# Optimization experiments

Measured on AMD Instinct MI355X. Metric: run time of the kernel, lower is better.

## Reference

```python
import jax, jax.numpy as jnp
import numpy as np

N_NODES = 100000


def gcn_conv(x, W, b, src, dst, n_nodes):
    # PyG GCNConv: h = x @ W; out = D^-1/2 (A + I) D^-1/2 h + b
    h = x @ W  # [N, F_out]
    e_ones = jnp.ones(src.shape[0], dtype=x.dtype)
    deg = jax.ops.segment_sum(e_ones, dst, num_segments=n_nodes) + 1.0  # self-loop
    dinv = jax.lax.rsqrt(deg)  # [N]
    norm = dinv[src] * dinv[dst]  # [E]
    msg = h[src] * norm[:, None]  # [E, F_out] (memory-bound gather)
    agg = jax.ops.segment_sum(msg, dst, num_segments=n_nodes)
    agg = agg + h * (dinv * dinv)[:, None]  # self-loop contribution
    return agg + b


def setup_inputs() -> dict:
    key = jax.random.key(0)
    ks = jax.random.split(key, 9)
    in_dim, h1, h2, out_dim = 512, 256, 128, 64
    n_edges = 1_600_000
    x = jax.random.normal(ks[0], (N_NODES, in_dim), dtype=jnp.float32)
    edge_index = jax.random.randint(ks[1], (2, n_edges), 0, N_NODES, dtype=jnp.int32)
    def glorot(k, fi, fo):
        s = float(np.sqrt(6.0 / (fi + fo)))
        return jax.random.uniform(k, (fi, fo), jnp.float32, -s, s)
    return {
        "x": x,
        "edge_index": edge_index,
        "W1": glorot(ks[2], in_dim, h1), "b1": jnp.zeros((h1,), jnp.float32),
        "W2": glorot(ks[3], h1, h2), "b2": jnp.zeros((h2,), jnp.float32),
        "W3": glorot(ks[4], h2, out_dim), "b3": jnp.zeros((out_dim,), jnp.float32),
    }


def reference(x, edge_index, W1, b1, W2, b2, W3, b3):
    src, dst = edge_index[0], edge_index[1]
    h = gcn_conv(x, W1, b1, src, dst, N_NODES)
    h = jax.nn.relu(h)  # dropout omitted (eval mode)
    h = gcn_conv(h, W2, b2, src, dst, N_NODES)
    h = jax.nn.relu(h)
    h = gcn_conv(h, W3, b3, src, dst, N_NODES)
    return jax.nn.log_softmax(h, axis=1)
```

## Files before the change

### kernel.cpp

```cpp
#include <hip/hip_runtime.h>
#include <hip/hip_bf16.h>

#define NN 100000
#define MP 100096

typedef unsigned short u16;
typedef __attribute__((ext_vector_type(8))) short bf16x8;
typedef __attribute__((ext_vector_type(4))) float f32x4;

static inline size_t align_up(size_t x, size_t a) { return (x + a - 1) & ~(a - 1); }

__device__ inline u16 f2b(float f) {
    unsigned u = __float_as_uint(f);
    return (u16)((u + 0x7FFF + ((u >> 16) & 1)) >> 16);
}
__device__ inline float b2f(u16 u) { return __uint_as_float(((unsigned)u) << 16); }


__global__ __launch_bounds__(256) void deg_count_kernel(const int* __restrict__ dst,
                                                        int* __restrict__ deg, int E) {
    int t = blockIdx.x * 256 + threadIdx.x;
    if (t < E) atomicAdd(&deg[dst[t]], 1);
}

__global__ __launch_bounds__(256) void dinv_kernel(const int* __restrict__ deg,
                                                   float* __restrict__ dinv, int n) {
    int t = blockIdx.x * 256 + threadIdx.x;
    if (t < n) dinv[t] = rsqrtf((float)deg[t] + 1.0f);
}

__global__ __launch_bounds__(256) void scan_phase1(const int* __restrict__ deg,
                                                   int* __restrict__ partials, int n4) {
    __shared__ int red[256];
    const int t = threadIdx.x;
    const int g = blockIdx.x * 256 + t;
    int4 v = make_int4(0, 0, 0, 0);
    if (g < n4) v = ((const int4*)deg)[g];
    red[t] = v.x + v.y + v.z + v.w;
    __syncthreads();
    #pragma unroll
    for (int d = 128; d; d >>= 1) {
        if (t < d) red[t] += red[t + d];
        __syncthreads();
    }
    if (t == 0) partials[blockIdx.x] = red[0];
}

__global__ __launch_bounds__(128) void scan_phase2(int* __restrict__ partials,
                                                   int* __restrict__ rowptr, int nb, int n) {
    __shared__ int ps[128];
    const int t = threadIdx.x;
    int v = (t < nb) ? partials[t] : 0;
    ps[t] = v;
    __syncthreads();
    #pragma unroll
    for (int d = 1; d < 128; d <<= 1) {
        int u = (t >= d) ? ps[t - d] : 0;
        __syncthreads();
        ps[t] += u;
        __syncthreads();
    }
    if (t < nb) partials[t] = ps[t] - v;
    if (t == nb - 1) rowptr[n] = ps[t];
}

__global__ __launch_bounds__(256) void scan_phase3(const int* __restrict__ deg,
                                                   const int* __restrict__ partials,
                                                   int* __restrict__ rowptr, int n4) {
    __shared__ int ts[256];
    const int t = threadIdx.x;
    const int g = blockIdx.x * 256 + t;
    int4 v = make_int4(0, 0, 0, 0);
    if (g < n4) v = ((const int4*)deg)[g];
    const int s0 = v.x, s1 = s0 + v.y, s2 = s1 + v.z, s3 = s2 + v.w;
    ts[t] = s3;
    __syncthreads();
    #pragma unroll
    for (int d = 1; d < 256; d <<= 1) {
        int u = (t >= d) ? ts[t - d] : 0;
        __syncthreads();
        ts[t] += u;
        __syncthreads();
    }
    if (g < n4) {
        const int base = partials[blockIdx.x] + ts[t] - s3;
        int4 r;
        r.x = base; r.y = base + s0; r.z = base + s1; r.w = base + s2;
        ((int4*)rowptr)[g] = r;
    }
}

__global__ __launch_bounds__(256) void reorder_kernel(const int* __restrict__ src,
        const int* __restrict__ dst, const int* __restrict__ rowptr,
        int* __restrict__ cursor, const float* __restrict__ dinv,
        int2* __restrict__ erec, int E) {
    int e = blockIdx.x * 256 + threadIdx.x;
    if (e >= E) return;
    int s = src[e], d = dst[e];
    int pos = rowptr[d] + atomicAdd(&cursor[d], 1);
    erec[pos] = make_int2(s, __float_as_int(dinv[s] * dinv[d]));
}


__global__ __launch_bounds__(256) void transpose_kernel(const float* __restrict__ W,
                                                        u16* __restrict__ WT, int K, int N) {
    int t = blockIdx.x * 256 + threadIdx.x;
    if (t >= K * N) return;
    int n = t / K, k = t - n * K;
    WT[t] = f2b(W[(size_t)k * N + n]);
}

__global__ __launch_bounds__(256) void gemm_mfma(const u16* __restrict__ A,
        const u16* __restrict__ BT, u16* __restrict__ C, int K, int ldc) {
    __shared__ char lds[32768];
    char* Al = lds;
    char* Bl = lds + 16384;
    const int tid = threadIdx.x;
    const int l = tid & 63;
    const int w = tid >> 6;
    const int wm = w >> 1, wn = w & 1;
    const long bm = (long)blockIdx.x * 128;
    const long bn = (long)blockIdx.y * 128;

    f32x4 acc[4][4];
    #pragma unroll
    for (int mi = 0; mi < 4; ++mi)
        #pragma unroll
        for (int ni = 0; ni < 4; ++ni)
            acc[mi][ni] = (f32x4){0.f, 0.f, 0.f, 0.f};

    const int srow = tid >> 3;
    const int schunk = (tid & 7) << 4;

    for (int k0 = 0; k0 < K; k0 += 64) {
        __syncthreads();
        #pragma unroll
        for (int i = 0; i < 4; ++i) {
            const int row = i * 32 + srow;
            const int lb = schunk ^ ((row & 7) << 4);
            const u16* ga = A + (bm + row) * K + k0 + (lb >> 1);
            const u16* gb = BT + (bn + row) * K + k0 + (lb >> 1);
            char* la = Al + i * 4096 + tid * 16;
            char* lbp = Bl + i * 4096 + tid * 16;
            __builtin_amdgcn_global_load_lds((const __attribute__((address_space(1))) void*)ga,
                                             (__attribute__((address_space(3))) void*)la, 16, 0, 0);
            __builtin_amdgcn_global_load_lds((const __attribute__((address_space(1))) void*)gb,
                                             (__attribute__((address_space(3))) void*)lbp, 16, 0, 0);
        }
        __syncthreads();
        #pragma unroll
        for (int kk = 0; kk < 2; ++kk) {
            const int kbyte = kk * 64 + ((l >> 4) << 4);
            const int swz = (l & 7) << 4;
            bf16x8 af[4], bfr[4];
            #pragma unroll
            for (int mi = 0; mi < 4; ++mi) {
                const int row = wm * 64 + mi * 16 + (l & 15);
                af[mi] = *(const bf16x8*)(Al + row * 128 + (kbyte ^ swz));
            }
            #pragma unroll
            for (int ni = 0; ni < 4; ++ni) {
                const int row = wn * 64 + ni * 16 + (l & 15);
                bfr[ni] = *(const bf16x8*)(Bl + row * 128 + (kbyte ^ swz));
            }
            #pragma unroll
            for (int mi = 0; mi < 4; ++mi)
                #pragma unroll
                for (int ni = 0; ni < 4; ++ni)
                    acc[mi][ni] = __builtin_amdgcn_mfma_f32_16x16x32_bf16(
                        af[mi], bfr[ni], acc[mi][ni], 0, 0, 0);
        }
    }

    const long r0 = bm + wm * 64 + ((l >> 4) << 2);
    const long c0 = bn + wn * 64 + (l & 15);
    #pragma unroll
    for (int mi = 0; mi < 4; ++mi)
        #pragma unroll
        for (int r = 0; r < 4; ++r) {
            const long row = r0 + mi * 16 + r;
            #pragma unroll
            for (int ni = 0; ni < 4; ++ni)
                C[row * ldc + c0 + ni * 16] = f2b(acc[mi][ni][r]);
        }
}

__global__ __launch_bounds__(256) void gemm_mfma_f32a(const float* __restrict__ A32,
        const u16* __restrict__ BT, u16* __restrict__ C, int K, int ldc) {
    __shared__ char lds[32768];
    char* Al = lds;
    char* Bl = lds + 16384;
    const int tid = threadIdx.x;
    const int l = tid & 63;
    const int w = tid >> 6;
    const int wm = w >> 1, wn = w & 1;
    const long bm = (long)blockIdx.x * 128;
    const long bn = (long)blockIdx.y * 128;

    f32x4 acc[4][4];
    #pragma unroll
    for (int mi = 0; mi < 4; ++mi)
        #pragma unroll
        for (int ni = 0; ni < 4; ++ni)
            acc[mi][ni] = (f32x4){0.f, 0.f, 0.f, 0.f};

    const int srow = tid >> 3;
    const int schunk = (tid & 7) << 4;

    for (int k0 = 0; k0 < K; k0 += 64) {
        __syncthreads();
        #pragma unroll
        for (int i = 0; i < 4; ++i) {
            const int row = i * 32 + srow;
            const int lb = schunk ^ ((row & 7) << 4);
            const u16* gb = BT + (bn + row) * K + k0 + (lb >> 1);
            char* lbp = Bl + i * 4096 + tid * 16;
            __builtin_amdgcn_global_load_lds((const __attribute__((address_space(1))) void*)gb,
                                             (__attribute__((address_space(3))) void*)lbp, 16, 0, 0);
        }
        float4 a0[4], a1[4];
        #pragma unroll
        for (int i = 0; i < 4; ++i) {
            const int row = i * 32 + srow;
            const long ar = (bm + row < NN) ? (bm + row) : (NN - 1);
            const float* ga = A32 + ar * K + k0 + (schunk >> 1);
            a0[i] = *(const float4*)ga;
            a1[i] = *(const float4*)(ga + 4);
        }
        #pragma unroll
        for (int i = 0; i < 4; ++i) {
            const int row = i * 32 + srow;
            bf16x8 v;
            v[0] = (short)f2b(a0[i].x); v[1] = (short)f2b(a0[i].y);
            v[2] = (short)f2b(a0[i].z); v[3] = (short)f2b(a0[i].w);
            v[4] = (short)f2b(a1[i].x); v[5] = (short)f2b(a1[i].y);
            v[6] = (short)f2b(a1[i].z); v[7] = (short)f2b(a1[i].w);
            *(bf16x8*)(Al + row * 128 + (schunk ^ ((row & 7) << 4))) = v;
        }
        __syncthreads();
        #pragma unroll
        for (int kk = 0; kk < 2; ++kk) {
            const int kbyte = kk * 64 + ((l >> 4) << 4);
            const int swz = (l & 7) << 4;
            bf16x8 af[4], bfr[4];
            #pragma unroll
            for (int mi = 0; mi < 4; ++mi) {
                const int row = wm * 64 + mi * 16 + (l & 15);
                af[mi] = *(const bf16x8*)(Al + row * 128 + (kbyte ^ swz));
            }
            #pragma unroll
            for (int ni = 0; ni < 4; ++ni) {
                const int row = wn * 64 + ni * 16 + (l & 15);
                bfr[ni] = *(const bf16x8*)(Bl + row * 128 + (kbyte ^ swz));
            }
            #pragma unroll
            for (int mi = 0; mi < 4; ++mi)
                #pragma unroll
                for (int ni = 0; ni < 4; ++ni)
                    acc[mi][ni] = __builtin_amdgcn_mfma_f32_16x16x32_bf16(
                        af[mi], bfr[ni], acc[mi][ni], 0, 0, 0);
        }
    }

    const long r0 = bm + wm * 64 + ((l >> 4) << 2);
    const long c0 = bn + wn * 64 + (l & 15);
    #pragma unroll
    for (int mi = 0; mi < 4; ++mi)
        #pragma unroll
        for (int r = 0; r < 4; ++r) {
            const long row = r0 + mi * 16 + r;
            #pragma unroll
            for (int ni = 0; ni < 4; ++ni)
                C[row * ldc + c0 + ni * 16] = f2b(acc[mi][ni][r]);
        }
}


template<int VEC, bool RELU>
__global__ __launch_bounds__(256) void agg_kernel(const u16* __restrict__ h,
        const int* __restrict__ rowptr, const int2* __restrict__ erec,
        const float* __restrict__ dinv, const float* __restrict__ bias,
        u16* __restrict__ out, int N) {
    const int node = blockIdx.x * 4 + (threadIdx.x >> 6);
    if (node >= N) return;
    const int lane = threadIdx.x & 63;
    const int F = 64 * VEC;
    const float di = dinv[node];
    const float d2 = di * di;
    float acc[VEC];
    {
        const u16* hp = h + (size_t)node * F + lane * VEC;
        if constexpr (VEC == 4) {
            ushort4 v = *(const ushort4*)hp;
            float4 b = *(const float4*)(bias + lane * 4);
            acc[0] = b2f(v.x) * d2 + b.x; acc[1] = b2f(v.y) * d2 + b.y;
            acc[2] = b2f(v.z) * d2 + b.z; acc[3] = b2f(v.w) * d2 + b.w;
        } else {
            ushort2 v = *(const ushort2*)hp;
            float2 b = *(const float2*)(bias + lane * 2);
            acc[0] = b2f(v.x) * d2 + b.x; acc[1] = b2f(v.y) * d2 + b.y;
        }
    }
    const int e0 = rowptr[node], e1 = rowptr[node + 1];
    int e = e0;
    for (; e + 8 <= e1; e += 8) {
        int2 r[8];
        #pragma unroll
        for (int j = 0; j < 8; ++j) r[j] = erec[e + j];
        if constexpr (VEC == 4) {
            ushort4 v[8];
            #pragma unroll
            for (int j = 0; j < 8; ++j)
                v[j] = *(const ushort4*)(h + (size_t)r[j].x * F + lane * 4);
            #pragma unroll
            for (int j = 0; j < 8; ++j) {
                const float wj = __int_as_float(r[j].y);
                acc[0] += b2f(v[j].x) * wj; acc[1] += b2f(v[j].y) * wj;
                acc[2] += b2f(v[j].z) * wj; acc[3] += b2f(v[j].w) * wj;
            }
        } else {
            ushort2 v[8];
            #pragma unroll
            for (int j = 0; j < 8; ++j)
                v[j] = *(const ushort2*)(h + (size_t)r[j].x * F + lane * 2);
            #pragma unroll
            for (int j = 0; j < 8; ++j) {
                const float wj = __int_as_float(r[j].y);
                acc[0] += b2f(v[j].x) * wj; acc[1] += b2f(v[j].y) * wj;
            }
        }
    }
    for (; e + 4 <= e1; e += 4) {
        int2 r[4];
        #pragma unroll
        for (int j = 0; j < 4; ++j) r[j] = erec[e + j];
        if constexpr (VEC == 4) {
            ushort4 v[4];
            #pragma unroll
            for (int j = 0; j < 4; ++j)
                v[j] = *(const ushort4*)(h + (size_t)r[j].x * F + lane * 4);
            #pragma unroll
            for (int j = 0; j < 4; ++j) {
                const float wj = __int_as_float(r[j].y);
                acc[0] += b2f(v[j].x) * wj; acc[1] += b2f(v[j].y) * wj;
                acc[2] += b2f(v[j].z) * wj; acc[3] += b2f(v[j].w) * wj;
            }
        } else {
            ushort2 v[4];
            #pragma unroll
            for (int j = 0; j < 4; ++j)
                v[j] = *(const ushort2*)(h + (size_t)r[j].x * F + lane * 2);
            #pragma unroll
            for (int j = 0; j < 4; ++j) {
                const float wj = __int_as_float(r[j].y);
                acc[0] += b2f(v[j].x) * wj; acc[1] += b2f(v[j].y) * wj;
            }
        }
    }
    for (; e < e1; ++e) {
        int2 r = erec[e];
        const float wgt = __int_as_float(r.y);
        const u16* sp = h + (size_t)r.x * F + lane * VEC;
        if constexpr (VEC == 4) {
            ushort4 v = *(const ushort4*)sp;
            acc[0] += b2f(v.x) * wgt; acc[1] += b2f(v.y) * wgt;
            acc[2] += b2f(v.z) * wgt; acc[3] += b2f(v.w) * wgt;
        } else {
            ushort2 v = *(const ushort2*)sp;
            acc[0] += b2f(v.x) * wgt; acc[1] += b2f(v.y) * wgt;
        }
    }
    u16* op = out + (size_t)node * F + lane * VEC;
    if constexpr (VEC == 4) {
        ushort4 r;
        r.x = f2b(RELU ? fmaxf(acc[0], 0.f) : acc[0]);
        r.y = f2b(RELU ? fmaxf(acc[1], 0.f) : acc[1]);
        r.z = f2b(RELU ? fmaxf(acc[2], 0.f) : acc[2]);
        r.w = f2b(RELU ? fmaxf(acc[3], 0.f) : acc[3]);
        *(ushort4*)op = r;
    } else {
        ushort2 r;
        r.x = f2b(RELU ? fmaxf(acc[0], 0.f) : acc[0]);
        r.y = f2b(RELU ? fmaxf(acc[1], 0.f) : acc[1]);
        *(ushort2*)op = r;
    }
}

__global__ __launch_bounds__(256) void agg_lsm_kernel(const u16* __restrict__ h,
        const int* __restrict__ rowptr, const int2* __restrict__ erec,
        const float* __restrict__ dinv, const float* __restrict__ bias,
        float* __restrict__ out, int N) {
    const int node = blockIdx.x * 4 + (threadIdx.x >> 6);
    if (node >= N) return;
    const int lane = threadIdx.x & 63;
    const float di = dinv[node];
    float acc = b2f(h[(size_t)node * 128 + lane]) * di * di + bias[lane];
    const int e0 = rowptr[node], e1 = rowptr[node + 1];
    int e = e0;
    for (; e + 8 <= e1; e += 8) {
        int2 r[8];
        #pragma unroll
        for (int j = 0; j < 8; ++j) r[j] = erec[e + j];
        float v[8];
        #pragma unroll
        for (int j = 0; j < 8; ++j) v[j] = b2f(h[(size_t)r[j].x * 128 + lane]);
        #pragma unroll
        for (int j = 0; j < 8; ++j) acc += v[j] * __int_as_float(r[j].y);
    }
    for (; e + 4 <= e1; e += 4) {
        int2 r[4];
        #pragma unroll
        for (int j = 0; j < 4; ++j) r[j] = erec[e + j];
        float v[4];
        #pragma unroll
        for (int j = 0; j < 4; ++j) v[j] = b2f(h[(size_t)r[j].x * 128 + lane]);
        #pragma unroll
        for (int j = 0; j < 4; ++j) acc += v[j] * __int_as_float(r[j].y);
    }
    for (; e < e1; ++e) {
        int2 r = erec[e];
        acc += b2f(h[(size_t)r.x * 128 + lane]) * __int_as_float(r.y);
    }
    float m = acc;
    #pragma unroll
    for (int o = 32; o; o >>= 1) m = fmaxf(m, __shfl_xor(m, o, 64));
    float ex = __expf(acc - m);
    float s = ex;
    #pragma unroll
    for (int o = 32; o; o >>= 1) s += __shfl_xor(s, o, 64);
    out[(size_t)node * 64 + lane] = acc - m - __logf(s);
}


extern "C" void kernel_launch(void* const* d_in, const int* in_sizes, int n_in,
                              void* d_out, int out_size, void* d_ws, size_t ws_size,
                              hipStream_t stream) {
    const float* x  = (const float*)d_in[0];
    const int*   ei = (const int*)d_in[1];
    const float* W1 = (const float*)d_in[2];
    const float* b1 = (const float*)d_in[3];
    const float* W2 = (const float*)d_in[4];
    const float* b2 = (const float*)d_in[5];
    const float* W3 = (const float*)d_in[6];
    const float* b3 = (const float*)d_in[7];
    const int E = in_sizes[1] / 2;
    const int* src = ei;
    const int* dst = ei + E;
    const int N = NN;
    const int N4 = N / 4;
    const int NB = (N4 + 255) / 256;

    char* ws = (char*)d_ws;
    int*   deg      = (int*)ws;    ws += align_up((size_t)N * 4, 256);
    int*   cursor   = (int*)ws;    ws += align_up((size_t)N * 4, 256);
    float* dinv     = (float*)ws;  ws += align_up((size_t)N * 4, 256);
    int*   rowptr   = (int*)ws;    ws += align_up((size_t)(N + 1) * 4, 256);
    int*   partials = (int*)ws;    ws += align_up((size_t)128 * 4, 256);
    int2*  erec     = (int2*)ws;   ws += align_up((size_t)E * 8, 256);
    u16*   wt1      = (u16*)ws;    ws += align_up((size_t)256 * 512 * 2, 256);
    u16*   wt2      = (u16*)ws;    ws += align_up((size_t)128 * 256 * 2, 256);
    u16*   wt3      = (u16*)ws;    ws += align_up((size_t)128 * 128 * 2, 256);
    u16*   bufH     = (u16*)ws;    ws += (size_t)MP * 256 * 2;
    u16*   bufAct   = (u16*)ws;    ws += (size_t)MP * 256 * 2;
    u16*   h2b      = (u16*)ws;    ws += (size_t)MP * 128 * 2;
    u16*   h3b  = bufH;
    float* out  = (float*)d_out;

    hipMemsetAsync(deg, 0, 2 * align_up((size_t)N * 4, 256), stream);

    deg_count_kernel<<<(E + 255) / 256, 256, 0, stream>>>(dst, deg, E);
    dinv_kernel<<<(N + 255) / 256, 256, 0, stream>>>(deg, dinv, N);
    scan_phase1<<<NB, 256, 0, stream>>>(deg, partials, N4);
    scan_phase2<<<1, 128, 0, stream>>>(partials, rowptr, NB, N);
    scan_phase3<<<NB, 256, 0, stream>>>(deg, partials, rowptr, N4);
    reorder_kernel<<<(E + 255) / 256, 256, 0, stream>>>(src, dst, rowptr, cursor, dinv, erec, E);

    transpose_kernel<<<(512 * 256 + 255) / 256, 256, 0, stream>>>(W1, wt1, 512, 256);
    transpose_kernel<<<(256 * 128 + 255) / 256, 256, 0, stream>>>(W2, wt2, 256, 128);
    transpose_kernel<<<(128 * 64 + 255) / 256, 256, 0, stream>>>(W3, wt3, 128, 64);

    const int GB = MP / 128;
    const int AB = (N + 3) / 4;

    gemm_mfma_f32a<<<dim3(GB, 2), 256, 0, stream>>>(x, wt1, bufH, 512, 256);
    agg_kernel<4, true><<<AB, 256, 0, stream>>>(bufH, rowptr, erec, dinv, b1, bufAct, N);

    gemm_mfma<<<dim3(GB, 1), 256, 0, stream>>>(bufAct, wt2, h2b, 256, 128);
    agg_kernel<2, true><<<AB, 256, 0, stream>>>(h2b, rowptr, erec, dinv, b2, bufAct, N);

    gemm_mfma<<<dim3(GB, 1), 256, 0, stream>>>(bufAct, wt3, h3b, 128, 128);
    agg_lsm_kernel<<<AB, 256, 0, stream>>>(h3b, rowptr, erec, dinv, b3, out, N);
}
```

Baseline: 773.6 us.

## Split layer-1 aggregation into feature slices and tighten layer-3 output width

The first-layer aggregation now runs as two passes over 128-column slices of the 256-wide hidden buffer, so each pass gathers a smaller per-node working set that may fit better in cache. The layer-3 GEMM writes only its 64 real columns, which halves the row stride the final aggregation gathers from. The dinv computation is fused into the first scan phase, and the three weight transposes become one launch. The 8-edge unrolled gather loops are removed, leaving 4-edge batches, which lowers register use but gives fewer loads in flight per edge batch. Splitting layer 1 also means the edge list and row pointers are read twice.

```diff
diff --git a/kernel.cpp b/kernel.cpp
--- a/kernel.cpp
+++ b/kernel.cpp
@@ -23,19 +23,22 @@
     if (t < E) atomicAdd(&deg[dst[t]], 1);
 }
 
-__global__ __launch_bounds__(256) void dinv_kernel(const int* __restrict__ deg,
-                                                   float* __restrict__ dinv, int n) {
-    int t = blockIdx.x * 256 + threadIdx.x;
-    if (t < n) dinv[t] = rsqrtf((float)deg[t] + 1.0f);
-}
-
 __global__ __launch_bounds__(256) void scan_phase1(const int* __restrict__ deg,
-                                                   int* __restrict__ partials, int n4) {
+                                                   int* __restrict__ partials,
+                                                   float* __restrict__ dinv, int n4) {
     __shared__ int red[256];
     const int t = threadIdx.x;
     const int g = blockIdx.x * 256 + t;
     int4 v = make_int4(0, 0, 0, 0);
-    if (g < n4) v = ((const int4*)deg)[g];
+    if (g < n4) {
+        v = ((const int4*)deg)[g];
+        float4 dv;
+        dv.x = rsqrtf((float)v.x + 1.0f);
+        dv.y = rsqrtf((float)v.y + 1.0f);
+        dv.z = rsqrtf((float)v.z + 1.0f);
+        dv.w = rsqrtf((float)v.w + 1.0f);
+        ((float4*)dinv)[g] = dv;
+    }
     red[t] = v.x + v.y + v.z + v.w;
     __syncthreads();
     #pragma unroll
@@ -101,17 +104,26 @@
     erec[pos] = make_int2(s, __float_as_int(dinv[s] * dinv[d]));
 }
 
-
-__global__ __launch_bounds__(256) void transpose_kernel(const float* __restrict__ W,
-                                                        u16* __restrict__ WT, int K, int N) {
+__global__ __launch_bounds__(256) void transpose_all(const float* __restrict__ W1,
+        const float* __restrict__ W2, const float* __restrict__ W3,
+        u16* __restrict__ wt1, u16* __restrict__ wt2, u16* __restrict__ wt3) {
     int t = blockIdx.x * 256 + threadIdx.x;
-    if (t >= K * N) return;
-    int n = t / K, k = t - n * K;
-    WT[t] = f2b(W[(size_t)k * N + n]);
+    if (t < 131072) {
+        int n = t >> 9, k = t & 511;
+        wt1[t] = f2b(W1[(size_t)k * 256 + n]);
+    } else if (t < 163840) {
+        int i = t - 131072;
+        int n = i >> 8, k = i & 255;
+        wt2[i] = f2b(W2[(size_t)k * 128 + n]);
+    } else if (t < 172032) {
+        int i = t - 163840;
+        int n = i >> 7, k = i & 127;
+        wt3[i] = f2b(W3[(size_t)k * 64 + n]);
+    }
 }
 
 __global__ __launch_bounds__(256) void gemm_mfma(const u16* __restrict__ A,
-        const u16* __restrict__ BT, u16* __restrict__ C, int K, int ldc) {
+        const u16* __restrict__ BT, u16* __restrict__ C, int K, int ldc, int ncols) {
     __shared__ char lds[32768];
     char* Al = lds;
     char* Bl = lds + 16384;
@@ -180,8 +192,10 @@
         for (int r = 0; r < 4; ++r) {
             const long row = r0 + mi * 16 + r;
             #pragma unroll
-            for (int ni = 0; ni < 4; ++ni)
-                C[row * ldc + c0 + ni * 16] = f2b(acc[mi][ni][r]);
+            for (int ni = 0; ni < 4; ++ni) {
+                const long c = c0 + ni * 16;
+                if (c < ncols) C[row * ldc + c] = f2b(acc[mi][ni][r]);
+            }
         }
 }
 
@@ -277,19 +291,18 @@
 
 
 template<int VEC, bool RELU>
-__global__ __launch_bounds__(256) void agg_kernel(const u16* __restrict__ h,
+__global__ __launch_bounds__(256) void agg_slice(const u16* __restrict__ h, int ldh,
         const int* __restrict__ rowptr, const int2* __restrict__ erec,
         const float* __restrict__ dinv, const float* __restrict__ bias,
-        u16* __restrict__ out, int N) {
+        u16* __restrict__ out, int ldo, int N) {
     const int node = blockIdx.x * 4 + (threadIdx.x >> 6);
     if (node >= N) return;
     const int lane = threadIdx.x & 63;
-    const int F = 64 * VEC;
     const float di = dinv[node];
     const float d2 = di * di;
     float acc[VEC];
     {
-        const u16* hp = h + (size_t)node * F + lane * VEC;
+        const u16* hp = h + (size_t)node * ldh + lane * VEC;
         if constexpr (VEC == 4) {
             ushort4 v = *(const ushort4*)hp;
             float4 b = *(const float4*)(bias + lane * 4);
@@ -303,33 +316,6 @@
     }
     const int e0 = rowptr[node], e1 = rowptr[node + 1];
     int e = e0;
-    for (; e + 8 <= e1; e += 8) {
-        int2 r[8];
-        #pragma unroll
-        for (int j = 0; j < 8; ++j) r[j] = erec[e + j];
-        if constexpr (VEC == 4) {
-            ushort4 v[8];
-            #pragma unroll
-            for (int j = 0; j < 8; ++j)
-                v[j] = *(const ushort4*)(h + (size_t)r[j].x * F + lane * 4);
-            #pragma unroll
-            for (int j = 0; j < 8; ++j) {
-                const float wj = __int_as_float(r[j].y);
-                acc[0] += b2f(v[j].x) * wj; acc[1] += b2f(v[j].y) * wj;
-                acc[2] += b2f(v[j].z) * wj; acc[3] += b2f(v[j].w) * wj;
-            }
-        } else {
-            ushort2 v[8];
-            #pragma unroll
-            for (int j = 0; j < 8; ++j)
-                v[j] = *(const ushort2*)(h + (size_t)r[j].x * F + lane * 2);
-            #pragma unroll
-            for (int j = 0; j < 8; ++j) {
-                const float wj = __int_as_float(r[j].y);
-                acc[0] += b2f(v[j].x) * wj; acc[1] += b2f(v[j].y) * wj;
-            }
-        }
-    }
     for (; e + 4 <= e1; e += 4) {
         int2 r[4];
         #pragma unroll
@@ -338,7 +324,7 @@
             ushort4 v[4];
             #pragma unroll
             for (int j = 0; j < 4; ++j)
-                v[j] = *(const ushort4*)(h + (size_t)r[j].x * F + lane * 4);
+                v[j] = *(const ushort4*)(h + (size_t)r[j].x * ldh + lane * 4);
             #pragma unroll
             for (int j = 0; j < 4; ++j) {
                 const float wj = __int_as_float(r[j].y);
@@ -349,7 +335,7 @@
             ushort2 v[4];
             #pragma unroll
             for (int j = 0; j < 4; ++j)
-                v[j] = *(const ushort2*)(h + (size_t)r[j].x * F + lane * 2);
+                v[j] = *(const ushort2*)(h + (size_t)r[j].x * ldh + lane * 2);
             #pragma unroll
             for (int j = 0; j < 4; ++j) {
                 const float wj = __int_as_float(r[j].y);
@@ -360,7 +346,7 @@
     for (; e < e1; ++e) {
         int2 r = erec[e];
         const float wgt = __int_as_float(r.y);
-        const u16* sp = h + (size_t)r.x * F + lane * VEC;
+        const u16* sp = h + (size_t)r.x * ldh + lane * VEC;
         if constexpr (VEC == 4) {
             ushort4 v = *(const ushort4*)sp;
             acc[0] += b2f(v.x) * wgt; acc[1] += b2f(v.y) * wgt;
@@ -370,7 +356,7 @@
             acc[0] += b2f(v.x) * wgt; acc[1] += b2f(v.y) * wgt;
         }
     }
-    u16* op = out + (size_t)node * F + lane * VEC;
+    u16* op = out + (size_t)node * ldo + lane * VEC;
     if constexpr (VEC == 4) {
         ushort4 r;
         r.x = f2b(RELU ? fmaxf(acc[0], 0.f) : acc[0]);
@@ -394,32 +380,22 @@
     if (node >= N) return;
     const int lane = threadIdx.x & 63;
     const float di = dinv[node];
-    float acc = b2f(h[(size_t)node * 128 + lane]) * di * di + bias[lane];
+    float acc = b2f(h[(size_t)node * 64 + lane]) * di * di + bias[lane];
     const int e0 = rowptr[node], e1 = rowptr[node + 1];
     int e = e0;
-    for (; e + 8 <= e1; e += 8) {
-        int2 r[8];
-        #pragma unroll
-        for (int j = 0; j < 8; ++j) r[j] = erec[e + j];
-        float v[8];
-        #pragma unroll
-        for (int j = 0; j < 8; ++j) v[j] = b2f(h[(size_t)r[j].x * 128 + lane]);
-        #pragma unroll
-        for (int j = 0; j < 8; ++j) acc += v[j] * __int_as_float(r[j].y);
-    }
     for (; e + 4 <= e1; e += 4) {
         int2 r[4];
         #pragma unroll
         for (int j = 0; j < 4; ++j) r[j] = erec[e + j];
         float v[4];
         #pragma unroll
-        for (int j = 0; j < 4; ++j) v[j] = b2f(h[(size_t)r[j].x * 128 + lane]);
+        for (int j = 0; j < 4; ++j) v[j] = b2f(h[(size_t)r[j].x * 64 + lane]);
         #pragma unroll
         for (int j = 0; j < 4; ++j) acc += v[j] * __int_as_float(r[j].y);
     }
     for (; e < e1; ++e) {
         int2 r = erec[e];
-        acc += b2f(h[(size_t)r.x * 128 + lane]) * __int_as_float(r.y);
+        acc += b2f(h[(size_t)r.x * 64 + lane]) * __int_as_float(r.y);
     }
     float m = acc;
     #pragma unroll
@@ -469,25 +445,23 @@
     hipMemsetAsync(deg, 0, 2 * align_up((size_t)N * 4, 256), stream);
 
     deg_count_kernel<<<(E + 255) / 256, 256, 0, stream>>>(dst, deg, E);
-    dinv_kernel<<<(N + 255) / 256, 256, 0, stream>>>(deg, dinv, N);
-    scan_phase1<<<NB, 256, 0, stream>>>(deg, partials, N4);
+    scan_phase1<<<NB, 256, 0, stream>>>(deg, partials, dinv, N4);
     scan_phase2<<<1, 128, 0, stream>>>(partials, rowptr, NB, N);
     scan_phase3<<<NB, 256, 0, stream>>>(deg, partials, rowptr, N4);
     reorder_kernel<<<(E + 255) / 256, 256, 0, stream>>>(src, dst, rowptr, cursor, dinv, erec, E);
 
-    transpose_kernel<<<(512 * 256 + 255) / 256, 256, 0, stream>>>(W1, wt1, 512, 256);
-    transpose_kernel<<<(256 * 128 + 255) / 256, 256, 0, stream>>>(W2, wt2, 256, 128);
-    transpose_kernel<<<(128 * 64 + 255) / 256, 256, 0, stream>>>(W3, wt3, 128, 64);
+    transpose_all<<<(172032 + 255) / 256, 256, 0, stream>>>(W1, W2, W3, wt1, wt2, wt3);
 
     const int GB = MP / 128;
     const int AB = (N + 3) / 4;
 
     gemm_mfma_f32a<<<dim3(GB, 2), 256, 0, stream>>>(x, wt1, bufH, 512, 256);
-    agg_kernel<4, true><<<AB, 256, 0, stream>>>(bufH, rowptr, erec, dinv, b1, bufAct, N);
-
-    gemm_mfma<<<dim3(GB, 1), 256, 0, stream>>>(bufAct, wt2, h2b, 256, 128);
-    agg_kernel<2, true><<<AB, 256, 0, stream>>>(h2b, rowptr, erec, dinv, b2, bufAct, N);
-
-    gemm_mfma<<<dim3(GB, 1), 256, 0, stream>>>(bufAct, wt3, h3b, 128, 128);
+    agg_slice<2, true><<<AB, 256, 0, stream>>>(bufH,       256, rowptr, erec, dinv, b1,       bufAct,       256, N);
+    agg_slice<2, true><<<AB, 256, 0, stream>>>(bufH + 128, 256, rowptr, erec, dinv, b1 + 128, bufAct + 128, 256, N);
+
+    gemm_mfma<<<dim3(GB, 1), 256, 0, stream>>>(bufAct, wt2, h2b, 256, 128, 128);
+    agg_slice<2, true><<<AB, 256, 0, stream>>>(h2b, 128, rowptr, erec, dinv, b2, bufAct, 128, N);
+
+    gemm_mfma<<<dim3(GB, 1), 256, 0, stream>>>(bufAct, wt3, h3b, 128, 64, 64);
     agg_lsm_kernel<<<AB, 256, 0, stream>>>(h3b, rowptr, erec, dinv, b3, out, N);
 }
```

Result: slower. 811.8 us (+4.9%).
